# Performance work log

Measured on AMD Instinct MI355X. Metric: run time of the kernel, lower is better.

Reference implementation:

```python
import jax, jax.numpy as jnp
import numpy as np

N = 50000      # nodes
E = 800000     # edges (avg degree 16)
IN, HID, OUT = 256, 128, 64
K, ALPHA = 4, 0.0  # APPNPConv(k=4, alpha=0.0)


def setup_inputs() -> dict:
    key = jax.random.key(0)
    ks = jax.random.split(key, 5)
    features = jax.random.normal(ks[0], (N, IN), jnp.float32)
    src = jax.random.randint(ks[1], (E,), 0, N, jnp.int32)
    dst = jax.random.randint(ks[2], (E,), 0, N, jnp.int32)
    W1 = jax.random.normal(ks[3], (IN, HID), jnp.float32) / np.float32(np.sqrt(IN))
    b1 = jnp.zeros((HID,), jnp.float32)
    W3 = jax.random.normal(ks[4], (HID, OUT), jnp.float32) / np.float32(np.sqrt(HID))
    b3 = jnp.zeros((OUT,), jnp.float32)
    return dict(features=features, src=src, dst=dst, W1=W1, b1=b1, W3=W3, b3=b3)


def _sym_norms(src, dst, n):
    # D_out^{-1/2} for source side, D_in^{-1/2} for destination side (DGL norm='both')
    ones = jnp.ones((src.shape[0],), jnp.float32)
    deg_out = jax.ops.segment_sum(ones, src, num_segments=n)
    deg_in = jax.ops.segment_sum(ones, dst, num_segments=n)
    return jnp.clip(deg_out, 1.0) ** -0.5, jnp.clip(deg_in, 1.0) ** -0.5


def _prop(x, src, dst, norm_src, norm_dst):
    # x: [N, D]. Symmetric-normalized SpMM: D_in^{-1/2} A D_out^{-1/2} x
    msg = (x * norm_src[:, None])[src]                       # [E, D] gather
    agg = jax.ops.segment_sum(msg, dst, num_segments=x.shape[0])  # [N, D] scatter-add
    return agg * norm_dst[:, None]


def reference(features, src, dst, W1, b1, W3, b3):
    ns, nd = _sym_norms(src, dst, N)
    # GraphConv 1 (weight-first since in_dim > hidden_dim; math identical either way)
    h = _prop(features @ W1, src, dst, ns, nd) + b1
    # dropout is identity in eval mode (training=False)
    # APPNPConv: k=4 power-iteration steps with teleport alpha=0.0
    h0 = h
    for _ in range(K):
        h = (1.0 - ALPHA) * _prop(h, src, dst, ns, nd) + ALPHA * h0
    # GraphConv 3
    out = _prop(h @ W3, src, dst, ns, nd) + b3
    return out
```

## Files before the change

kernel.cpp:

```cpp
#include <hip/hip_runtime.h>
#include <math.h>

#define N_NODES 50000
#define N_EDGES 800000
#define DIN 256
#define DHID 128
#define DOUT 64
#define CSTRIDE 64
#define ZROW N_NODES
#define HBLOCKS 256
#define HCHUNK (N_EDGES / HBLOCKS)
#define HWORDS (N_NODES / 4)
#define SLICE ((size_t)(N_NODES + 1) * 16)
#define NGROUPS (N_NODES / 4)
#define P2BLOCKS 196

#define SB_SENT 3125
#define SB_HS (SB_SENT + HBLOCKS)
#define SB_HD (SB_HS + HBLOCKS)
#define SB_TOT (SB_HD + 66)

__global__ void k_setup(const int* __restrict__ src, const int* __restrict__ dst,
                        unsigned int* __restrict__ pS, unsigned int* __restrict__ pD,
                        unsigned int* __restrict__ csr32,
                        const float* __restrict__ W1, const float* __restrict__ b1,
                        const float* __restrict__ W3,
                        float* __restrict__ W13, float* __restrict__ bb,
                        float* __restrict__ Y0, float* __restrict__ Y1) {
    __shared__ unsigned int h[HWORDS];
    int bx = blockIdx.x, t = threadIdx.x;
    if (bx < SB_SENT) {
        unsigned int v = (unsigned int)ZROW | ((unsigned int)ZROW << 16);
        uint2 o; o.x = v; o.y = v;
        ((uint2*)csr32)[bx * 256 + t] = o;
        return;
    }
    if (bx < SB_HD) {
        const int* idx = (bx < SB_HS) ? src : dst;
        unsigned int* outp = (bx < SB_HS) ? pS : pD;
        int hb = bx - ((bx < SB_HS) ? SB_SENT : SB_HS);
        for (int w = t; w < HWORDS; w += 256) h[w] = 0u;
        __syncthreads();
        int base = hb * HCHUNK;
        for (int i = t; i < HCHUNK; i += 256) {
            int s = idx[base + i];
            atomicAdd(&h[s >> 2], 1u << ((s & 3) << 3));
        }
        __syncthreads();
        outp += (size_t)hb * HWORDS;
        for (int w = t; w < HWORDS; w += 256) outp[w] = h[w];
        return;
    }
    int vb = bx - SB_HD;
    if (vb == 65) {
        if (t < 64) {
            int qq = t >> 4, c2 = t & 15;
            Y0[(size_t)qq * SLICE + ((size_t)ZROW << 4) + c2] = 0.f;
            Y1[(size_t)qq * SLICE + ((size_t)ZROW << 4) + c2] = 0.f;
        }
        return;
    }
    if (vb == 64) {
        if (t < DOUT) {
            float s = 0.f;
            for (int k = 0; k < DHID; ++k) s += b1[k] * W3[k * DOUT + t];
            bb[t] = s;
        }
        return;
    }
    int idx2 = vb * 256 + t;
    int i = idx2 >> 6, j = idx2 & 63;
    float s = 0.f;
    for (int k = 0; k < DHID; ++k) s += W1[i * DHID + k] * W3[k * DOUT + j];
    W13[idx2] = s;
}

__global__ void k_hpre(const unsigned int* __restrict__ pS,
                       const unsigned int* __restrict__ pD,
                       unsigned int* __restrict__ prefix,
                       int* __restrict__ deg_in,
                       float* __restrict__ ns, float* __restrict__ nd,
                       float* __restrict__ cc, int* __restrict__ dparts) {
    __shared__ unsigned int sdw[64][4];
    __shared__ unsigned int sow[64][4];
    __shared__ int lh[65];
    int t = threadIdx.x;
    if (t < 65) lh[t] = 0;
    int col = t >> 2, sub = t & 3;
    int wid = blockIdx.x * 64 + col;
    bool act = wid < HWORDS;
    unsigned int ps = 0, pd = 0;
    if (act) {
        int b0 = sub << 6;
#pragma unroll 4
        for (int b = b0; b < b0 + 64; ++b) {
            ps += pS[(size_t)b * HWORDS + wid];
            pd += pD[(size_t)b * HWORDS + wid];
        }
    }
    sdw[col][sub] = pd;
    sow[col][sub] = ps;
    __syncthreads();
    if (act) {
        unsigned int base = 0;
        for (int k = 0; k < sub; ++k) base += sdw[col][k];
        int b0 = sub << 6;
        unsigned int run = base;
        for (int b = b0; b < b0 + 64; ++b) {
            unsigned int w = pD[(size_t)b * HWORDS + wid];
            prefix[(size_t)b * HWORDS + wid] = run;
            run += w;
        }
        if (sub == 0) {
            unsigned int totd = sdw[col][0] + sdw[col][1] + sdw[col][2] + sdw[col][3];
            unsigned int toto = sow[col][0] + sow[col][1] + sow[col][2] + sow[col][3];
            unsigned int di[4] = {totd & 0xffu, (totd >> 8) & 0xffu,
                                  (totd >> 16) & 0xffu, totd >> 24};
            unsigned int dov[4] = {toto & 0xffu, (toto >> 8) & 0xffu,
                                   (toto >> 16) & 0xffu, toto >> 24};
            int4 dd; dd.x = (int)di[0]; dd.y = (int)di[1]; dd.z = (int)di[2]; dd.w = (int)di[3];
            *(int4*)(deg_in + (wid << 2)) = dd;
            float4 vns, vnd, vcc;
            float* pns = &vns.x; float* pnd = &vnd.x; float* pcc = &vcc.x;
#pragma unroll
            for (int q = 0; q < 4; ++q) {
                int bin = (int)di[q]; if (bin > 64) bin = 64;
                atomicAdd(&lh[bin], 1);
                unsigned int a = dov[q] < 1u ? 1u : dov[q];
                unsigned int b = di[q] < 1u ? 1u : di[q];
                float fa = 1.0f / sqrtf((float)a);
                float fb = 1.0f / sqrtf((float)b);
                pns[q] = fa; pnd[q] = fb; pcc[q] = fa * fb;
            }
            *(float4*)(ns + (wid << 2)) = vns;
            *(float4*)(nd + (wid << 2)) = vnd;
            *(float4*)(cc + (wid << 2)) = vcc;
        }
    }
    __syncthreads();
    if (t < 65) dparts[blockIdx.x * 65 + t] = lh[t];
}

__global__ void k_dscan(const int* __restrict__ dparts, int* __restrict__ offs) {
    __shared__ int colsum[65], binbase[65];
    int t = threadIdx.x;
    if (t < 65) {
        int s = 0;
        for (int b = 0; b < P2BLOCKS; ++b) s += dparts[b * 65 + t];
        colsum[t] = s;
    }
    __syncthreads();
    if (t == 0) {
        int run = 0;
        for (int k = 64; k >= 0; --k) { binbase[k] = run; run += colsum[k]; }
    }
    __syncthreads();
    if (t < 65) {
        int run = binbase[t];
        for (int b = 0; b < P2BLOCKS; ++b) { offs[b * 65 + t] = run; run += dparts[b * 65 + t]; }
    }
}

__global__ void k_dscatter(const int* __restrict__ deg_in, const int* __restrict__ offs,
                           const float* __restrict__ cc, const float* __restrict__ ns,
                           const float* __restrict__ nd,
                           int* __restrict__ perm, int* __restrict__ inv,
                           int* __restrict__ degP, float* __restrict__ ccP,
                           float* __restrict__ nsP, float* __restrict__ ndP) {
    __shared__ int off[65];
    int t = threadIdx.x;
    if (t < 65) off[t] = offs[blockIdx.x * 65 + t];
    __syncthreads();
    int wid = blockIdx.x * 64 + t;
    if (t < 64 && wid < HWORDS) {
        int4 d4 = *(const int4*)(deg_in + (wid << 2));
        int dd[4] = {d4.x, d4.y, d4.z, d4.w};
#pragma unroll
        for (int k = 0; k < 4; ++k) {
            int node = (wid << 2) + k;
            int bin = dd[k] > 64 ? 64 : dd[k];
            int slot = atomicAdd(&off[bin], 1);
            perm[slot] = node; inv[node] = slot;
            degP[slot] = dd[k];
            ccP[slot] = cc[node]; nsP[slot] = ns[node]; ndP[slot] = nd[node];
        }
    }
}

__global__ void k_fill(const int* __restrict__ src, const int* __restrict__ dst,
                       const unsigned int* __restrict__ prefix,
                       const int* __restrict__ inv,
                       unsigned short* __restrict__ csr) {
    __shared__ unsigned int h[HWORDS];
    int t = threadIdx.x;
    const unsigned int* prow = prefix + (size_t)blockIdx.x * HWORDS;
    for (int w = t; w < HWORDS; w += 256) h[w] = prow[w];
    __syncthreads();
    int base = blockIdx.x * HCHUNK;
    for (int i = t; i < HCHUNK; i += 256) {
        int s = src[base + i], d = dst[base + i];
        int sh = (d & 3) << 3;
        unsigned int old = atomicAdd(&h[d >> 2], 1u << sh);
        int slot = (int)((old >> sh) & 0xffu);
        csr[((size_t)inv[d] << 6) + slot] = (unsigned short)inv[s];
    }
}

__global__ void k_gemm(const float* __restrict__ X, const float* __restrict__ W13,
                       const float* __restrict__ ns, const int* __restrict__ inv,
                       float* __restrict__ Y) {
    __shared__ float As[16][34];
    __shared__ float Bs[16][64];
    int tid = threadIdx.x;
    int tx = tid & 15, ty = tid >> 4;
    int row0 = blockIdx.x * 32;
    float acc[2][4];
#pragma unroll
    for (int i = 0; i < 2; ++i)
#pragma unroll
        for (int j = 0; j < 4; ++j) acc[i][j] = 0.f;

    int lr = tid & 31;
    int lk2 = (tid >> 5) << 1;
    int arow = row0 + lr;
    if (arow > N_NODES - 1) arow = N_NODES - 1;

    for (int k0 = 0; k0 < DIN; k0 += 16) {
        float2 a = *(const float2*)(X + (size_t)arow * DIN + k0 + lk2);
        As[lk2][lr] = a.x; As[lk2 + 1][lr] = a.y;
        float4 b = *(const float4*)(W13 + (size_t)(k0 + ty) * DOUT + (tx << 2));
        *(float4*)&Bs[ty][tx << 2] = b;
        __syncthreads();
#pragma unroll
        for (int k = 0; k < 16; ++k) {
            float2 av = *(const float2*)&As[k][ty << 1];
            float4 bv = *(const float4*)&Bs[k][tx << 2];
            float ar[2] = {av.x, av.y};
            float br[4] = {bv.x, bv.y, bv.z, bv.w};
#pragma unroll
            for (int i = 0; i < 2; ++i)
#pragma unroll
                for (int j = 0; j < 4; ++j) acc[i][j] += ar[i] * br[j];
        }
        __syncthreads();
    }
    int qq = tx >> 2;
    int co = (tx & 3) << 2;
#pragma unroll
    for (int i = 0; i < 2; ++i) {
        int row = row0 + (ty << 1) + i;
        if (row < N_NODES) {
            float nsr = ns[row];
            int prow = inv[row];
            float4 o;
            o.x = acc[i][0] * nsr; o.y = acc[i][1] * nsr;
            o.z = acc[i][2] * nsr; o.w = acc[i][3] * nsr;
            *(float4*)(Y + (size_t)qq * SLICE + ((size_t)prow << 4) + co) = o;
        }
    }
}


template <int MODE>
__launch_bounds__(256, 8)
__global__ void k_spmm(const float* __restrict__ xs, float* __restrict__ ys,
                       const unsigned short* __restrict__ csr,
                       const int* __restrict__ degP,
                       const float* __restrict__ ccP, const float* __restrict__ nsP,
                       const float* __restrict__ ndP,
                       const float* __restrict__ bb, const float* __restrict__ b3,
                       const int* __restrict__ perm) {
    __shared__ unsigned short rows[4][256];
    int wid  = threadIdx.x >> 6;
    int lane = threadIdx.x & 63;
    int q    = (blockIdx.x & 7) >> 1;
    int half = blockIdx.x & 1;
    int g    = (blockIdx.x >> 3) * 8 + wid * 2 + half;
    if (g >= NGROUPS) return;
    int node0 = g << 2;

    int nn = lane >> 4, sl = lane & 15;
    const uint2* crow = (const uint2*)(csr + ((size_t)(node0 + nn) << 6)) + sl;
    uint2 rv = *crow;
    unsigned short* bp = &rows[wid][(sl << 4) + nn];
    bp[0]  = (unsigned short)(rv.x & 0xffffu);
    bp[4]  = (unsigned short)(rv.x >> 16);
    bp[8]  = (unsigned short)(rv.y & 0xffffu);
    bp[12] = (unsigned short)(rv.y >> 16);

    int n0u = __builtin_amdgcn_readfirstlane(node0);
    int m = (degP[n0u] + 3) & ~3;

    int n = lane >> 4, e = (lane >> 2) & 3, c4 = lane & 3;
    const unsigned short* rd = &rows[wid][(e << 2) + n];
    const float* xq = xs + (size_t)q * SLICE + (c4 << 2);

    float ax = 0.f, ay = 0.f, az = 0.f, aw = 0.f;
#define LDV(T) const float4 v##T = *(const float4*)(xq + ((size_t)rd[16 * (T)] << 4))
#define ACCV(T) ax += v##T.x; ay += v##T.y; az += v##T.z; aw += v##T.w
    if (m <= 4) {
        LDV(0); ACCV(0);
    } else if (m <= 8) {
        LDV(0); LDV(1);
        ACCV(0); ACCV(1);
    } else if (m <= 12) {
        LDV(0); LDV(1); LDV(2);
        ACCV(0); ACCV(1); ACCV(2);
    } else if (m <= 16) {
        LDV(0); LDV(1); LDV(2); LDV(3);
        ACCV(0); ACCV(1); ACCV(2); ACCV(3);
    } else if (m <= 20) {
        LDV(0); LDV(1); LDV(2); LDV(3); LDV(4);
        ACCV(0); ACCV(1); ACCV(2); ACCV(3); ACCV(4);
    } else if (m <= 24) {
        LDV(0); LDV(1); LDV(2); LDV(3); LDV(4); LDV(5);
        ACCV(0); ACCV(1); ACCV(2); ACCV(3); ACCV(4); ACCV(5);
    } else if (m <= 28) {
        LDV(0); LDV(1); LDV(2); LDV(3); LDV(4); LDV(5); LDV(6);
        ACCV(0); ACCV(1); ACCV(2); ACCV(3); ACCV(4); ACCV(5); ACCV(6);
    } else if (m <= 32) {
        LDV(0); LDV(1); LDV(2); LDV(3); LDV(4); LDV(5); LDV(6); LDV(7);
        ACCV(0); ACCV(1); ACCV(2); ACCV(3); ACCV(4); ACCV(5); ACCV(6); ACCV(7);
    } else {
        for (int j2 = 0; j2 < m; j2 += 4) {
            const float4 a = *(const float4*)(xq + ((size_t)rd[j2 << 2] << 4));
            ax += a.x; ay += a.y; az += a.z; aw += a.w;
        }
    }
#undef LDV
#undef ACCV
    ax += __shfl_xor(ax, 4);  ay += __shfl_xor(ay, 4);
    az += __shfl_xor(az, 4);  aw += __shfl_xor(aw, 4);
    ax += __shfl_xor(ax, 8);  ay += __shfl_xor(ay, 8);
    az += __shfl_xor(az, 8);  aw += __shfl_xor(aw, 8);

    int nodeL = node0 + n;
    int colq  = (q << 4) + (c4 << 2);
    float4 r;
    if (MODE == 0) {
        float cv = ccP[nodeL], nv = nsP[nodeL];
        float4 bv = *(const float4*)(bb + colq);
        r.x = cv * ax + nv * bv.x; r.y = cv * ay + nv * bv.y;
        r.z = cv * az + nv * bv.z; r.w = cv * aw + nv * bv.w;
    } else if (MODE == 1) {
        float cv = ccP[nodeL];
        r.x = cv * ax; r.y = cv * ay; r.z = cv * az; r.w = cv * aw;
    } else {
        float dv = ndP[nodeL];
        float4 bv = *(const float4*)(b3 + colq);
        r.x = dv * ax + bv.x; r.y = dv * ay + bv.y;
        r.z = dv * az + bv.z; r.w = dv * aw + bv.w;
    }
    if (e == 0) {
        if (MODE == 2) {
            int orow = perm[nodeL];
            *(float4*)(ys + ((size_t)orow << 6) + colq) = r;
        } else {
            *(float4*)(ys + (size_t)q * SLICE + ((size_t)nodeL << 4) + (c4 << 2)) = r;
        }
    }
}


extern "C" void kernel_launch(void* const* d_in, const int* in_sizes, int n_in,
                              void* d_out, int out_size, void* d_ws, size_t ws_size,
                              hipStream_t stream) {
    const float* X   = (const float*)d_in[0];
    const int*   src = (const int*)d_in[1];
    const int*   dst = (const int*)d_in[2];
    const float* W1  = (const float*)d_in[3];
    const float* b1  = (const float*)d_in[4];
    const float* W3  = (const float*)d_in[5];
    const float* b3  = (const float*)d_in[6];
    float* out = (float*)d_out;

    char* ws = (char*)d_ws;
    size_t off = 0;
    auto alloc = [&](size_t bytes) -> void* {
        void* p = ws + off;
        off = (off + bytes + 255) & ~(size_t)255;
        return p;
    };
    unsigned int*   pS     = (unsigned int*)alloc((size_t)HBLOCKS * HWORDS * 4);
    unsigned int*   pD     = (unsigned int*)alloc((size_t)HBLOCKS * HWORDS * 4);
    unsigned int*   pref   = (unsigned int*)alloc((size_t)HBLOCKS * HWORDS * 4);
    float*          Y0     = (float*)alloc(SLICE * 4 * 4);
    float*          Y1     = (float*)alloc(SLICE * 4 * 4);
    unsigned short* csr    = (unsigned short*)alloc((size_t)N_NODES * CSTRIDE * 2);
    int*            deg_in = (int*)alloc((size_t)N_NODES * 4);
    float*          ns     = (float*)alloc((size_t)N_NODES * 4);
    float*          nd     = (float*)alloc((size_t)N_NODES * 4);
    float*          cc     = (float*)alloc((size_t)N_NODES * 4);
    int*            perm   = (int*)alloc((size_t)N_NODES * 4);
    int*            inv    = (int*)alloc((size_t)N_NODES * 4);
    int*            degP   = (int*)alloc((size_t)N_NODES * 4);
    float*          ccP    = (float*)alloc((size_t)N_NODES * 4);
    float*          nsP    = (float*)alloc((size_t)N_NODES * 4);
    float*          ndP    = (float*)alloc((size_t)N_NODES * 4);
    int*            dparts = (int*)alloc((size_t)P2BLOCKS * 65 * 4);
    int*            offs   = (int*)alloc((size_t)P2BLOCKS * 65 * 4);
    float*          W13    = (float*)alloc((size_t)DIN * DOUT * 4);
    float*          bb     = (float*)alloc(DOUT * 4);

    const int sblk = 1563 * 8;

    k_setup<<<SB_TOT, 256, 0, stream>>>(src, dst, pS, pD, (unsigned int*)csr,
                                        W1, b1, W3, W13, bb, Y0, Y1);
    k_hpre<<<P2BLOCKS, 256, 0, stream>>>(pS, pD, pref, deg_in, ns, nd, cc, dparts);
    k_dscan<<<1, 128, 0, stream>>>(dparts, offs);
    k_dscatter<<<P2BLOCKS, 128, 0, stream>>>(deg_in, offs, cc, ns, nd,
                                             perm, inv, degP, ccP, nsP, ndP);
    k_fill<<<HBLOCKS, 256, 0, stream>>>(src, dst, pref, inv, csr);

    k_gemm<<<(N_NODES + 31) / 32, 256, 0, stream>>>(X, W13, ns, inv, Y0);

    k_spmm<0><<<sblk, 256, 0, stream>>>(Y0, Y1, csr, degP, ccP, nsP, ndP, bb, b3, perm);
    k_spmm<1><<<sblk, 256, 0, stream>>>(Y1, Y0, csr, degP, ccP, nsP, ndP, bb, b3, perm);
    k_spmm<1><<<sblk, 256, 0, stream>>>(Y0, Y1, csr, degP, ccP, nsP, ndP, bb, b3, perm);
    k_spmm<1><<<sblk, 256, 0, stream>>>(Y1, Y0, csr, degP, ccP, nsP, ndP, bb, b3, perm);
    k_spmm<1><<<sblk, 256, 0, stream>>>(Y0, Y1, csr, degP, ccP, nsP, ndP, bb, b3, perm);
    k_spmm<2><<<sblk, 256, 0, stream>>>(Y1, out, csr, degP, ccP, nsP, ndP, bb, b3, perm);
}
```

Baseline: 313.6 us.

## Restructure GEMM to stage half of W in LDS and stream X rows from registers

The GEMM kernel now loads a 128x64 half of the combined weight matrix into shared memory at a time. Each of four threads per row reads that row of X straight from global memory with float4 loads and accumulates a 16-column output strip, replacing the old 16-wide K-tiled shared-memory scheme with frequent barriers. Each block covers 64 rows instead of 32, which removes most barrier and X-staging overhead. The cost is uncoalesced strided X reads, since the four threads of a row read the same address and adjacent rows are 1KB apart, plus more LDS traffic per FMA.

```diff
diff --git a/kernel.cpp b/kernel.cpp
--- a/kernel.cpp
+++ b/kernel.cpp
@@ -209,54 +209,68 @@
 __global__ void k_gemm(const float* __restrict__ X, const float* __restrict__ W13,
                        const float* __restrict__ ns, const int* __restrict__ inv,
                        float* __restrict__ Y) {
-    __shared__ float As[16][34];
-    __shared__ float Bs[16][64];
+    __shared__ float Ws[128][64];
     int tid = threadIdx.x;
-    int tx = tid & 15, ty = tid >> 4;
-    int row0 = blockIdx.x * 32;
-    float acc[2][4];
-#pragma unroll
-    for (int i = 0; i < 2; ++i)
-#pragma unroll
-        for (int j = 0; j < 4; ++j) acc[i][j] = 0.f;
-
-    int lr = tid & 31;
-    int lk2 = (tid >> 5) << 1;
-    int arow = row0 + lr;
-    if (arow > N_NODES - 1) arow = N_NODES - 1;
-
-    for (int k0 = 0; k0 < DIN; k0 += 16) {
-        float2 a = *(const float2*)(X + (size_t)arow * DIN + k0 + lk2);
-        As[lk2][lr] = a.x; As[lk2 + 1][lr] = a.y;
-        float4 b = *(const float4*)(W13 + (size_t)(k0 + ty) * DOUT + (tx << 2));
-        *(float4*)&Bs[ty][tx << 2] = b;
+    int r = tid >> 2;
+    int cq = tid & 3;
+    int row = blockIdx.x * 64 + r;
+    if (row > N_NODES - 1) row = N_NODES - 1;
+    const float* xr = X + (size_t)row * DIN;
+
+    float4 a0 = {0,0,0,0}, a1 = {0,0,0,0}, a2 = {0,0,0,0}, a3 = {0,0,0,0};
+
+#define FMA4(XV, KROW)                                                     \
+    do {                                                                   \
+        float xv_ = (XV);                                                  \
+        const float* wr_ = &Ws[(KROW)][cq << 4];                           \
+        float4 w0_ = *(const float4*)(wr_);                                \
+        float4 w1_ = *(const float4*)(wr_ + 4);                            \
+        float4 w2_ = *(const float4*)(wr_ + 8);                            \
+        float4 w3_ = *(const float4*)(wr_ + 12);                           \
+        a0.x += xv_ * w0_.x; a0.y += xv_ * w0_.y;                          \
+        a0.z += xv_ * w0_.z; a0.w += xv_ * w0_.w;                          \
+        a1.x += xv_ * w1_.x; a1.y += xv_ * w1_.y;                          \
+        a1.z += xv_ * w1_.z; a1.w += xv_ * w1_.w;                          \
+        a2.x += xv_ * w2_.x; a2.y += xv_ * w2_.y;                          \
+        a2.z += xv_ * w2_.z; a2.w += xv_ * w2_.w;                          \
+        a3.x += xv_ * w3_.x; a3.y += xv_ * w3_.y;                          \
+        a3.z += xv_ * w3_.z; a3.w += xv_ * w3_.w;                          \
+    } while (0)
+
+    for (int h = 0; h < 2; ++h) {
         __syncthreads();
-#pragma unroll
-        for (int k = 0; k < 16; ++k) {
-            float2 av = *(const float2*)&As[k][ty << 1];
-            float4 bv = *(const float4*)&Bs[k][tx << 2];
-            float ar[2] = {av.x, av.y};
-            float br[4] = {bv.x, bv.y, bv.z, bv.w};
-#pragma unroll
-            for (int i = 0; i < 2; ++i)
-#pragma unroll
-                for (int j = 0; j < 4; ++j) acc[i][j] += ar[i] * br[j];
+        {
+            const float4* wsrc = (const float4*)(W13 + (size_t)h * 128 * DOUT);
+            float4* wdst = (float4*)&Ws[0][0];
+            for (int i = tid; i < 2048; i += 256) wdst[i] = wsrc[i];
         }
         __syncthreads();
-    }
-    int qq = tx >> 2;
-    int co = (tx & 3) << 2;
-#pragma unroll
-    for (int i = 0; i < 2; ++i) {
-        int row = row0 + (ty << 1) + i;
-        if (row < N_NODES) {
-            float nsr = ns[row];
-            int prow = inv[row];
-            float4 o;
-            o.x = acc[i][0] * nsr; o.y = acc[i][1] * nsr;
-            o.z = acc[i][2] * nsr; o.w = acc[i][3] * nsr;
-            *(float4*)(Y + (size_t)qq * SLICE + ((size_t)prow << 4) + co) = o;
-        }
+        const float* xh = xr + (h << 7);
+        for (int k0 = 0; k0 < 128; k0 += 8) {
+            float4 xa = *(const float4*)(xh + k0);
+            float4 xb = *(const float4*)(xh + k0 + 4);
+            FMA4(xa.x, k0 + 0); FMA4(xa.y, k0 + 1);
+            FMA4(xa.z, k0 + 2); FMA4(xa.w, k0 + 3);
+            FMA4(xb.x, k0 + 4); FMA4(xb.y, k0 + 5);
+            FMA4(xb.z, k0 + 6); FMA4(xb.w, k0 + 7);
+        }
+    }
+#undef FMA4
+
+    int orow = blockIdx.x * 64 + r;
+    if (orow < N_NODES) {
+        float nsr = ns[orow];
+        int prow = inv[orow];
+        float* yp = Y + (size_t)cq * SLICE + ((size_t)prow << 4);
+        float4 o;
+        o.x = a0.x * nsr; o.y = a0.y * nsr; o.z = a0.z * nsr; o.w = a0.w * nsr;
+        *(float4*)(yp) = o;
+        o.x = a1.x * nsr; o.y = a1.y * nsr; o.z = a1.z * nsr; o.w = a1.w * nsr;
+        *(float4*)(yp + 4) = o;
+        o.x = a2.x * nsr; o.y = a2.y * nsr; o.z = a2.z * nsr; o.w = a2.w * nsr;
+        *(float4*)(yp + 8) = o;
+        o.x = a3.x * nsr; o.y = a3.y * nsr; o.z = a3.z * nsr; o.w = a3.w * nsr;
+        *(float4*)(yp + 12) = o;
     }
 }
 
@@ -412,7 +426,7 @@
                                              perm, inv, degP, ccP, nsP, ndP);
     k_fill<<<HBLOCKS, 256, 0, stream>>>(src, dst, pref, inv, csr);
 
-    k_gemm<<<(N_NODES + 31) / 32, 256, 0, stream>>>(X, W13, ns, inv, Y0);
+    k_gemm<<<(N_NODES + 63) / 64, 256, 0, stream>>>(X, W13, ns, inv, Y0);
 
     k_spmm<0><<<sblk, 256, 0, stream>>>(Y0, Y1, csr, degP, ccP, nsP, ndP, bb, b3, perm);
     k_spmm<1><<<sblk, 256, 0, stream>>>(Y1, Y0, csr, degP, ccP, nsP, ndP, bb, b3, perm);
```

Measured after the change: 315.7 us. About the same (+0.7%).
